# Kernel tuning notes

Measured on AMD Instinct MI355X. Metric: run time of the kernel, lower is better.

## Reference

```python
import jax, jax.numpy as jnp
import numpy as np

B, T, C = 8, 1024, 1024
NH, HD = 16, 64          # num_heads, head_dim (C = NH*HD)
NL = 8                   # num_layers
TPB = 64                 # tokens_per_block (block_causal)
EPS = 1e-5


def setup_inputs() -> dict:
    key = jax.random.key(0)
    ks = jax.random.split(key, 12)
    s = 0.02
    sequences = jax.random.normal(ks[0], (B, T, C), dtype=jnp.float32)
    # block-causal mask: causal OR same-block (tril | block_diag)
    idx = jnp.arange(T)
    mask = (idx[:, None] >= idx[None, :]) | ((idx[:, None] // TPB) == (idx[None, :] // TPB))
    # stacked per-layer params; torch Linear convention: W has shape [out, in]
    d = {
        "sequences": sequences,
        "mask": mask,
        "Wq": jax.random.normal(ks[1], (NL, C, C)) * s, "bq": jnp.zeros((NL, C)),
        "Wk": jax.random.normal(ks[2], (NL, C, C)) * s, "bk": jnp.zeros((NL, C)),
        "Wv": jax.random.normal(ks[3], (NL, C, C)) * s, "bv": jnp.zeros((NL, C)),
        "Wo": jax.random.normal(ks[4], (NL, C, C)) * s, "bo": jnp.zeros((NL, C)),
        "ln1w": jnp.ones((NL, C)), "ln1b": jnp.zeros((NL, C)),
        "ln2w": jnp.ones((NL, C)), "ln2b": jnp.zeros((NL, C)),
        "W1": jax.random.normal(ks[5], (NL, 4 * C, C)) * s, "b1": jnp.zeros((NL, 4 * C)),
        "W2": jax.random.normal(ks[6], (NL, C, 4 * C)) * s, "b2": jnp.zeros((NL, C)),
        "lnfw": jnp.ones((C,)), "lnfb": jnp.zeros((C,)),
    }
    return d


def _layernorm(x, w, b):
    m = jnp.mean(x, axis=-1, keepdims=True)
    v = jnp.mean(jnp.square(x - m), axis=-1, keepdims=True)
    return (x - m) * jax.lax.rsqrt(v + EPS) * w + b


def _linear(x, W, b):  # x: [..., in], W: [out, in]
    return jnp.einsum('...i,oi->...o', x, W) + b


def _attention(h, mask, Wq, bq, Wk, bk, Wv, bv, Wo, bo):
    # h: [B,T,C]
    q = _linear(h, Wq, bq).reshape(B, T, NH, HD)
    k = _linear(h, Wk, bk).reshape(B, T, NH, HD)
    v = _linear(h, Wv, bv).reshape(B, T, NH, HD)
    att = jnp.einsum('bqhd,bkhd->bhqk', q, k) * (HD ** -0.5)
    att = jnp.where(mask, att, -jnp.inf)
    att = jax.nn.softmax(att, axis=-1)
    y = jnp.einsum('bhqk,bkhd->bqhd', att, v).reshape(B, T, C)
    return _linear(y, Wo, bo)


def reference(sequences, mask, Wq, bq, Wk, bk, Wv, bv, Wo, bo,
              ln1w, ln1b, ln2w, ln2b, W1, b1, W2, b2, lnfw, lnfb):
    x = sequences  # dropout p=0
    for i in range(NL):
        h = _layernorm(x, ln1w[i], ln1b[i])
        x = x + _attention(h, mask, Wq[i], bq[i], Wk[i], bk[i], Wv[i], bv[i], Wo[i], bo[i])
        h = _layernorm(x, ln2w[i], ln2b[i])
        h = _linear(h, W1[i], b1[i])
        h = jax.nn.gelu(h, approximate=False)  # torch nn.GELU default = exact erf
        x = x + _linear(h, W2[i], b2[i])
    return _layernorm(x, lnfw, lnfb)
```

## Files before the change

kernel.cpp:

```cpp
#include <hip/hip_runtime.h>
#include <math.h>

typedef unsigned short ushort_t;
typedef __attribute__((ext_vector_type(4))) float f32x4;
typedef __attribute__((ext_vector_type(8))) short short8;

constexpr int BATCH = 8, T = 1024, C = 1024, NH = 16, HD = 64, NL = 8;
constexpr int MROWS = BATCH * T;
constexpr int CS = 3 * C;

#define WAITVM(n) asm volatile("s_waitcnt vmcnt(" #n ")" ::: "memory")

__device__ __forceinline__ ushort_t f2bf(float f) {
  unsigned u = __builtin_bit_cast(unsigned, f);
  u += 0x7fffu + ((u >> 16) & 1u);
  return (ushort_t)(u >> 16);
}

__device__ __forceinline__ void gload_lds16(const ushort_t* g, ushort_t* l) {
  __builtin_amdgcn_global_load_lds(
      (const __attribute__((address_space(1))) unsigned int*)g,
      (__attribute__((address_space(3))) unsigned int*)l, 16, 0, 0);
}

__global__ __launch_bounds__(256, 8)
void convw_kernel(const float* __restrict__ Wq, const float* __restrict__ Wk,
                  const float* __restrict__ Wv, const float* __restrict__ Wo,
                  const float* __restrict__ W1, const float* __restrict__ W2,
                  const float* __restrict__ bq, const float* __restrict__ bk,
                  const float* __restrict__ bv,
                  ushort_t* __restrict__ wqkv, ushort_t* __restrict__ wo,
                  ushort_t* __restrict__ w1, ushort_t* __restrict__ w2,
                  float* __restrict__ bqkv)
{
  if (blockIdx.x == 6144) {
    int t = threadIdx.x;
    if (t < 384) {
      const float* s = (t < 128) ? (bq + t * 8)
                     : (t < 256) ? (bk + (t - 128) * 8)
                                 : (bv + (t - 256) * 8);
      f32x4 a = ((const f32x4*)s)[0], b = ((const f32x4*)s)[1];
      ((f32x4*)(bqkv + t * 8))[0] = a;
      ((f32x4*)(bqkv + t * 8))[1] = b;
    }
    return;
  }
  int g = blockIdx.x * 256 + threadIdx.x;
  const float* src;
  ushort_t* dst;
  if (g < 393216) {
    int which = g >> 17;
    int r = g & 131071;
    src = (which == 0 ? Wq : which == 1 ? Wk : Wv) + (size_t)r * 8;
    dst = wqkv + (size_t)g * 8;
  } else if (g < 524288) {
    int r = g - 393216;
    src = Wo + (size_t)r * 8; dst = wo + (size_t)r * 8;
  } else if (g < 1048576) {
    int r = g - 524288;
    src = W1 + (size_t)r * 8; dst = w1 + (size_t)r * 8;
  } else {
    int r = g - 1048576;
    src = W2 + (size_t)r * 8; dst = w2 + (size_t)r * 8;
  }
  f32x4 a = ((const f32x4*)src)[0], b = ((const f32x4*)src)[1];
  short8 o;
#pragma unroll
  for (int e = 0; e < 4; ++e) { o[e] = (short)f2bf(a[e]); o[e + 4] = (short)f2bf(b[e]); }
  *(short8*)dst = o;
}

template<int MODE, int NB>
__global__ __launch_bounds__(512, 1)
void gemmk(const ushort_t* __restrict__ A, const ushort_t* __restrict__ Wb,
           const float* __restrict__ bias, ushort_t* __restrict__ outb,
           float* __restrict__ resid, int K, int N, int nbn)
{
  constexpr int MI = (NB == 256) ? 8 : 4;
  constexpr int NI = 4;
  constexpr int WAVE_M = MI * 16;
  constexpr int NBJ = (NB == 256) ? 2 : 1;
  constexpr int AT = 256 * 32;
  constexpr int BT = NB * 32;

  __shared__ __align__(16) ushort_t As[4 * AT];
  __shared__ __align__(16) ushort_t Bs[4 * BT];

  const int tid = threadIdx.x;
  const int lane = tid & 63, wave = tid >> 6;
  const int wm = (NB == 256) ? (wave >> 2) : (wave >> 1);
  const int wn = (NB == 256) ? (wave & 3) : (wave & 1);
  const int l15 = lane & 15, l4 = lane >> 4;

  const int cpx = gridDim.x >> 3;
  const int xcd = blockIdx.x & 7;
  const int local = blockIdx.x >> 3;
  const int bm = xcd * 4 + local / nbn;
  const int bn = local % nbn;
  const long bm0 = (long)bm * 256;
  const long bn0 = (long)bn * NB;

  const ushort_t* srcA[2]; int dA[2];
#pragma unroll
  for (int j = 0; j < 2; ++j) {
    int cidx = j * 512 + tid;
    int row = cidx >> 2, c = cidx & 3;
    int cl = (c - (row >> 1)) & 3;
    srcA[j] = A + (size_t)(bm0 + row) * K + cl * 8;
    dA[j] = cidx * 8;
  }
  const ushort_t* srcB[NBJ]; int dB[NBJ];
#pragma unroll
  for (int j = 0; j < NBJ; ++j) {
    int cidx = j * 512 + tid;
    int row = cidx >> 2, c = cidx & 3;
    int cl = (c - (row >> 1)) & 3;
    srcB[j] = Wb + (size_t)(bn0 + row) * K + cl * 8;
    dB[j] = cidx * 8;
  }

  int aoff[MI], boff[NI];
#pragma unroll
  for (int mi = 0; mi < MI; ++mi) {
    int row = wm * WAVE_M + mi * 16 + l15;
    int p = (l4 + (row >> 1)) & 3;
    aoff[mi] = row * 32 + p * 8;
  }
#pragma unroll
  for (int ni = 0; ni < NI; ++ni) {
    int row = wn * 64 + ni * 16 + l15;
    int p = (l4 + (row >> 1)) & 3;
    boff[ni] = row * 32 + p * 8;
  }

  auto stage = [&](int buf, int kt) {
#pragma unroll
    for (int j = 0; j < 2; ++j)
      gload_lds16(srcA[j] + kt, &As[buf * AT + dA[j]]);
#pragma unroll
    for (int j = 0; j < NBJ; ++j)
      gload_lds16(srcB[j] + kt, &Bs[buf * BT + dB[j]]);
  };

  f32x4 acc[MI][NI] = {};
  const int nt = K >> 5;

  stage(0, 0); stage(1, 32); stage(2, 64);
  if (NB == 256) WAITVM(8); else WAITVM(6);
  __builtin_amdgcn_s_barrier();

  for (int t = 0; t < nt; ++t) {
    const ushort_t* Ab = &As[(t & 3) * AT];
    const ushort_t* Bb = &Bs[(t & 3) * BT];
    short8 af[MI], bf[NI];
#pragma unroll
    for (int mi = 0; mi < MI; ++mi) af[mi] = *(const short8*)&Ab[aoff[mi]];
#pragma unroll
    for (int ni = 0; ni < NI; ++ni) bf[ni] = *(const short8*)&Bb[boff[ni]];

    if (t + 3 < nt) stage((t + 3) & 3, (t + 3) << 5);
    __builtin_amdgcn_sched_barrier(0);

    __builtin_amdgcn_s_setprio(1);
#pragma unroll
    for (int mi = 0; mi < MI; ++mi)
#pragma unroll
      for (int ni = 0; ni < NI; ++ni)
        acc[mi][ni] = __builtin_amdgcn_mfma_f32_16x16x32_bf16(
            af[mi], bf[ni], acc[mi][ni], 0, 0, 0);
    __builtin_amdgcn_s_setprio(0);

    const int rem2 = nt - 2 - t;
    if (rem2 >= 2)      { if (NB == 256) WAITVM(8); else WAITVM(6); }
    else if (rem2 == 1) { if (NB == 256) WAITVM(4); else WAITVM(3); }
    else if (rem2 == 0) { WAITVM(0); }
    __builtin_amdgcn_s_barrier();
  }

#pragma unroll
  for (int ni = 0; ni < NI; ++ni) {
    long col = bn0 + wn * 64 + ni * 16 + l15;
    float bv = bias[col];
#pragma unroll
    for (int mi = 0; mi < MI; ++mi) {
#pragma unroll
      for (int r = 0; r < 4; ++r) {
        long row = bm0 + wm * WAVE_M + mi * 16 + l4 * 4 + r;
        float v = acc[mi][ni][r] + bv;
        if (MODE == 1) v = 0.5f * v * (1.0f + erff(v * 0.70710678118f));
        if (MODE == 2) {
          float* rp = resid + (size_t)row * N + col;
          *rp = *rp + v;
        } else {
          outb[(size_t)row * N + col] = f2bf(v);
        }
      }
    }
  }
}

__global__ __launch_bounds__(256, 4)
void attn_kernel(const ushort_t* __restrict__ qkv, ushort_t* __restrict__ y)
{
  __shared__ __align__(16) ushort_t Qs[64 * 64];
  __shared__ __align__(16) ushort_t Ks[64 * 64];
  __shared__ __align__(16) ushort_t Vts[64 * 64];
  __shared__ __align__(16) ushort_t Ps[64 * 64];
  const int tid = threadIdx.x;
  const int lane = tid & 63, wave = tid >> 6;
  const int l15 = lane & 15, l4 = lane >> 4;
  const int w16 = wave * 16;
  const int bid = blockIdx.x;
  const int pair = bid & 127, qb = bid >> 7;
  const int h = pair & 15, b = pair >> 4;
  const int qoff = h * HD, koff = C + h * HD, voff = 2 * C + h * HD;
  const size_t qrow0 = (size_t)(b * T + qb * 64);

#pragma unroll
  for (int j = 0; j < 2; ++j) {
    int cidx = j * 256 + tid;
    int row = cidx >> 3, cl = (cidx & 7) ^ (row & 7);
    gload_lds16(qkv + (qrow0 + row) * CS + qoff + cl * 8, &Qs[cidx * 8]);
  }

  f32x4 o[4] = {};
  float mrun[4] = {-INFINITY, -INFINITY, -INFINITY, -INFINITY};
  float lrun[4] = {0.f, 0.f, 0.f, 0.f};

  __syncthreads();

  for (int kvb = 0; kvb <= qb; ++kvb) {
    const size_t krow0 = (size_t)(b * T + kvb * 64);
#pragma unroll
    for (int j = 0; j < 2; ++j) {
      int cidx = j * 256 + tid;
      int row = cidx >> 3, cl = (cidx & 7) ^ (row & 7);
      gload_lds16(qkv + (krow0 + row) * CS + koff + cl * 8, &Ks[cidx * 8]);
    }
#pragma unroll
    for (int pass = 0; pass < 2; ++pass) {
      int dc = (tid >> 6) + pass * 4;
      int kvr = tid & 63;
      const ushort_t* src = qkv + (krow0 + kvr) * CS + voff + dc * 8;
      short8 vv = *(const short8*)src;
#pragma unroll
      for (int i = 0; i < 8; ++i) {
        int d = dc * 8 + i;
        Vts[d * 64 + (((kvr >> 3) ^ (d & 7)) << 3) + (kvr & 7)] = (ushort_t)vv[i];
      }
    }
    __syncthreads();

    f32x4 s[4] = {};
#pragma unroll
    for (int ks = 0; ks < 2; ++ks) {
      int arow = w16 + l15;
      int pa = (ks * 4 + l4) ^ (arow & 7);
      short8 aq = *(const short8*)&Qs[arow * 64 + pa * 8];
#pragma unroll
      for (int n = 0; n < 4; ++n) {
        int br = n * 16 + l15;
        int pb = (ks * 4 + l4) ^ (br & 7);
        short8 bk2 = *(const short8*)&Ks[br * 64 + pb * 8];
        s[n] = __builtin_amdgcn_mfma_f32_16x16x32_bf16(aq, bk2, s[n], 0, 0, 0);
      }
    }

#pragma unroll
    for (int r = 0; r < 4; ++r) {
      float mx = fmaxf(fmaxf(s[0][r], s[1][r]), fmaxf(s[2][r], s[3][r]));
#pragma unroll
      for (int d = 1; d < 16; d <<= 1) mx = fmaxf(mx, __shfl_xor(mx, d, 16));
      mx *= 0.125f;
      float mnew = fmaxf(mrun[r], mx);
      float alpha = __expf(mrun[r] - mnew);
      float rowsum = 0.f;
      int qr = w16 + l4 * 4 + r;
#pragma unroll
      for (int n = 0; n < 4; ++n) {
        float pv = __expf(s[n][r] * 0.125f - mnew);
        rowsum += pv;
        int kv = n * 16 + l15;
        Ps[qr * 64 + (((kv >> 3) ^ (qr & 7)) << 3) + (kv & 7)] = f2bf(pv);
      }
#pragma unroll
      for (int d = 1; d < 16; d <<= 1) rowsum += __shfl_xor(rowsum, d, 16);
      mrun[r] = mnew;
      lrun[r] = lrun[r] * alpha + rowsum;
      o[0][r] *= alpha; o[1][r] *= alpha; o[2][r] *= alpha; o[3][r] *= alpha;
    }

#pragma unroll
    for (int ks = 0; ks < 2; ++ks) {
      int arow = w16 + l15;
      int pa = (ks * 4 + l4) ^ (arow & 7);
      short8 ap = *(const short8*)&Ps[arow * 64 + pa * 8];
#pragma unroll
      for (int n = 0; n < 4; ++n) {
        int vr = n * 16 + l15;
        int pb = (ks * 4 + l4) ^ (vr & 7);
        short8 bvv = *(const short8*)&Vts[vr * 64 + pb * 8];
        o[n] = __builtin_amdgcn_mfma_f32_16x16x32_bf16(ap, bvv, o[n], 0, 0, 0);
      }
    }
    __syncthreads();
  }

#pragma unroll
  for (int n = 0; n < 4; ++n) {
#pragma unroll
    for (int r = 0; r < 4; ++r) {
      float val = o[n][r] / lrun[r];
      y[(qrow0 + w16 + l4 * 4 + r) * C + h * HD + n * 16 + l15] = f2bf(val);
    }
  }
}

template<int OUTBF16>
__global__ __launch_bounds__(256, 4)
void ln_kernel(const float* __restrict__ x, const float* __restrict__ w,
               const float* __restrict__ bprm, void* __restrict__ out)
{
  const size_t row = blockIdx.x;
  const int tid = threadIdx.x;
  f32x4 xv = ((const f32x4*)(x + row * 1024))[tid];
  float s1 = xv[0] + xv[1] + xv[2] + xv[3];
  float s2 = xv[0] * xv[0] + xv[1] * xv[1] + xv[2] * xv[2] + xv[3] * xv[3];
#pragma unroll
  for (int m = 1; m < 64; m <<= 1) {
    s1 += __shfl_xor(s1, m);
    s2 += __shfl_xor(s2, m);
  }
  __shared__ float red[8];
  const int wave = tid >> 6, lane = tid & 63;
  if (lane == 0) { red[wave * 2] = s1; red[wave * 2 + 1] = s2; }
  __syncthreads();
  s1 = red[0] + red[2] + red[4] + red[6];
  s2 = red[1] + red[3] + red[5] + red[7];
  const float mean = s1 * (1.f / 1024.f);
  const float var = s2 * (1.f / 1024.f) - mean * mean;
  const float rstd = rsqrtf(var + 1e-5f);
  f32x4 wv = ((const f32x4*)w)[tid];
  f32x4 bv = ((const f32x4*)bprm)[tid];
  f32x4 ov;
#pragma unroll
  for (int c2 = 0; c2 < 4; ++c2) ov[c2] = (xv[c2] - mean) * rstd * wv[c2] + bv[c2];
  if (OUTBF16) {
    ushort4 u;
    u.x = f2bf(ov[0]); u.y = f2bf(ov[1]); u.z = f2bf(ov[2]); u.w = f2bf(ov[3]);
    ((ushort4*)out)[row * 256 + tid] = u;
  } else {
    ((f32x4*)out)[row * 256 + tid] = ov;
  }
}

extern "C" void kernel_launch(void* const* d_in, const int* in_sizes, int n_in,
                              void* d_out, int out_size, void* d_ws, size_t ws_size,
                              hipStream_t stream)
{
  const float* seq  = (const float*)d_in[0];
  const float* Wq   = (const float*)d_in[2];  const float* bq = (const float*)d_in[3];
  const float* Wk   = (const float*)d_in[4];  const float* bk = (const float*)d_in[5];
  const float* Wv   = (const float*)d_in[6];  const float* bv = (const float*)d_in[7];
  const float* Wo   = (const float*)d_in[8];  const float* bo = (const float*)d_in[9];
  const float* ln1w = (const float*)d_in[10]; const float* ln1b = (const float*)d_in[11];
  const float* ln2w = (const float*)d_in[12]; const float* ln2b = (const float*)d_in[13];
  const float* W1   = (const float*)d_in[14]; const float* b1 = (const float*)d_in[15];
  const float* W2   = (const float*)d_in[16]; const float* b2 = (const float*)d_in[17];
  const float* lnfw = (const float*)d_in[18]; const float* lnfb = (const float*)d_in[19];

  char* ws = (char*)d_ws;
  size_t off = 0;
  float* X = (float*)(ws + off);         off += (size_t)MROWS * C * 4;
  ushort_t* Hb = (ushort_t*)(ws + off);  off += (size_t)MROWS * C * 2;
  ushort_t* Yb = (ushort_t*)(ws + off);  off += (size_t)MROWS * C * 2;
  ushort_t* BIG = (ushort_t*)(ws + off); off += (size_t)MROWS * 4 * C * 2;
  ushort_t* wqkv = (ushort_t*)(ws + off); off += (size_t)3 * C * C * 2;
  ushort_t* wo   = (ushort_t*)(ws + off); off += (size_t)C * C * 2;
  ushort_t* w1   = (ushort_t*)(ws + off); off += (size_t)4 * C * C * 2;
  ushort_t* w2   = (ushort_t*)(ws + off); off += (size_t)4 * C * C * 2;
  float* bqkv = (float*)(ws + off);       off += (size_t)3 * C * 4;
  ushort_t* QKVb = BIG;
  ushort_t* Gb = BIG;

  hipMemcpyAsync(X, seq, (size_t)MROWS * C * 4, hipMemcpyDeviceToDevice, stream);

  const dim3 blk(256);
  const dim3 blk512(512);
  const dim3 gQKV(384);
  const dim3 gN1024(256);
  const dim3 gN4096(512);
  const dim3 gAttn(2048);
  const dim3 gConv(6145);

  for (int i = 0; i < NL; ++i) {
    const size_t w1Off = (size_t)i * C * C;
    const size_t w4Off = (size_t)i * 4 * C * C;
    convw_kernel<<<gConv, blk, 0, stream>>>(Wq + w1Off, Wk + w1Off, Wv + w1Off,
                                            Wo + w1Off, W1 + w4Off, W2 + w4Off,
                                            bq + i * C, bk + i * C, bv + i * C,
                                            wqkv, wo, w1, w2, bqkv);
    ln_kernel<1><<<MROWS, blk, 0, stream>>>(X, ln1w + i * C, ln1b + i * C, Hb);
    gemmk<0, 256><<<gQKV, blk512, 0, stream>>>(Hb, wqkv, bqkv, QKVb, nullptr, C, CS, 12);
    attn_kernel<<<gAttn, blk, 0, stream>>>(QKVb, Yb);
    gemmk<2, 128><<<gN1024, blk512, 0, stream>>>(Yb, wo, bo + i * C, nullptr, X, C, C, 8);
    ln_kernel<1><<<MROWS, blk, 0, stream>>>(X, ln2w + i * C, ln2b + i * C, Hb);
    gemmk<1, 256><<<gN4096, blk512, 0, stream>>>(Hb, w1, b1 + (size_t)i * 4 * C, Gb, nullptr, C, 4 * C, 16);
    gemmk<2, 128><<<gN1024, blk512, 0, stream>>>(Gb, w2, b2 + i * C, nullptr, X, 4 * C, C, 8);
  }
  ln_kernel<0><<<MROWS, blk, 0, stream>>>(X, lnfw, lnfb, (float*)d_out);
}
```

Measured before the change: 3.200 ms.

## Restructure GEMM into 8-phase ping-pong pipeline with LDS-staged vectorized epilogue

Replaces the 4-stage single-phase GEMM loop with a K=64 double-buffered schedule split into four interleaved load/MFMA phases separated by barriers and priority hints, so LDS reads, global-to-LDS staging and MFMA overlap more finely. Tiles change to 256-wide N with BM of 128 or 256, and occupancy is raised to 2 blocks per CU. The epilogue now transposes accumulators through LDS to emit 16-byte vectorized stores and residual updates instead of scalar strided writes. The extra barriers add synchronisation overhead, and the larger LDS footprint and register pressure may limit the intended occupancy.

```diff
diff --git a/kernel.cpp b/kernel.cpp
--- a/kernel.cpp
+++ b/kernel.cpp
@@ -9,7 +9,9 @@
 constexpr int MROWS = BATCH * T;
 constexpr int CS = 3 * C;
 
-#define WAITVM(n) asm volatile("s_waitcnt vmcnt(" #n ")" ::: "memory")
+#define WAITVM0 asm volatile("s_waitcnt vmcnt(0)" ::: "memory")
+#define WAITVM4 asm volatile("s_waitcnt vmcnt(4)" ::: "memory")
+#define WAITVM6 asm volatile("s_waitcnt vmcnt(6)" ::: "memory")
 
 __device__ __forceinline__ ushort_t f2bf(float f) {
   unsigned u = __builtin_bit_cast(unsigned, f);
@@ -70,48 +72,47 @@
   *(short8*)dst = o;
 }
 
-template<int MODE, int NB>
-__global__ __launch_bounds__(512, 1)
-void gemmk(const ushort_t* __restrict__ A, const ushort_t* __restrict__ Wb,
-           const float* __restrict__ bias, ushort_t* __restrict__ outb,
-           float* __restrict__ resid, int K, int N, int nbn)
+template<int MODE, int BM>
+__global__ __launch_bounds__(512, 2)
+void gemm8p(const ushort_t* __restrict__ A, const ushort_t* __restrict__ Wb,
+            const float* __restrict__ bias, ushort_t* __restrict__ outb,
+            float* __restrict__ resid, int K, int N, int nbn)
 {
-  constexpr int MI = (NB == 256) ? 8 : 4;
-  constexpr int NI = 4;
-  constexpr int WAVE_M = MI * 16;
-  constexpr int NBJ = (NB == 256) ? 2 : 1;
-  constexpr int AT = 256 * 32;
-  constexpr int BT = NB * 32;
-
-  __shared__ __align__(16) ushort_t As[4 * AT];
-  __shared__ __align__(16) ushort_t Bs[4 * BT];
+  constexpr int MI = BM / 32;
+  constexpr int LA = BM / 128;
+  constexpr int AKH = BM * 32;
+  constexpr int ABUF = 2 * AKH;
+  constexpr int BKH = 256 * 32;
+  constexpr int BBUF = 2 * BKH;
+  constexpr int BMT = 8192 / BM;
+
+  __shared__ __align__(16) ushort_t As[2 * ABUF];
+  __shared__ __align__(16) ushort_t Bs[2 * BBUF];
 
   const int tid = threadIdx.x;
   const int lane = tid & 63, wave = tid >> 6;
-  const int wm = (NB == 256) ? (wave >> 2) : (wave >> 1);
-  const int wn = (NB == 256) ? (wave & 3) : (wave & 1);
+  const int wm = wave >> 2, wn = wave & 3;
   const int l15 = lane & 15, l4 = lane >> 4;
 
-  const int cpx = gridDim.x >> 3;
   const int xcd = blockIdx.x & 7;
   const int local = blockIdx.x >> 3;
-  const int bm = xcd * 4 + local / nbn;
+  const int bm = xcd * (BMT / 8) + local / nbn;
   const int bn = local % nbn;
-  const long bm0 = (long)bm * 256;
-  const long bn0 = (long)bn * NB;
-
-  const ushort_t* srcA[2]; int dA[2];
-#pragma unroll
-  for (int j = 0; j < 2; ++j) {
+  const long bm0 = (long)bm * BM;
+  const long bn0 = (long)bn * 256;
+
+  const ushort_t* srcA[LA]; int dA[LA];
+#pragma unroll
+  for (int j = 0; j < LA; ++j) {
     int cidx = j * 512 + tid;
     int row = cidx >> 2, c = cidx & 3;
     int cl = (c - (row >> 1)) & 3;
     srcA[j] = A + (size_t)(bm0 + row) * K + cl * 8;
     dA[j] = cidx * 8;
   }
-  const ushort_t* srcB[NBJ]; int dB[NBJ];
-#pragma unroll
-  for (int j = 0; j < NBJ; ++j) {
+  const ushort_t* srcB[2]; int dB[2];
+#pragma unroll
+  for (int j = 0; j < 2; ++j) {
     int cidx = j * 512 + tid;
     int row = cidx >> 2, c = cidx & 3;
     int cl = (c - (row >> 1)) & 3;
@@ -119,81 +120,156 @@
     dB[j] = cidx * 8;
   }
 
-  int aoff[MI], boff[NI];
+  auto stage_unit = [&](int u) {
+    int tau = u >> 2, part = u & 3;
+    int buf = tau & 1, kh = part >> 1;
+    int kt = (tau << 6) + (kh << 5);
+    if (part & 1) {
+#pragma unroll
+      for (int j = 0; j < 2; ++j)
+        gload_lds16(srcB[j] + kt, &Bs[buf * BBUF + kh * BKH + dB[j]]);
+    } else {
+#pragma unroll
+      for (int j = 0; j < LA; ++j)
+        gload_lds16(srcA[j] + kt, &As[buf * ABUF + kh * AKH + dA[j]]);
+    }
+  };
+
+  int aoffs[MI], boffs[4];
 #pragma unroll
   for (int mi = 0; mi < MI; ++mi) {
-    int row = wm * WAVE_M + mi * 16 + l15;
-    int p = (l4 + (row >> 1)) & 3;
-    aoff[mi] = row * 32 + p * 8;
-  }
-#pragma unroll
-  for (int ni = 0; ni < NI; ++ni) {
+    int row = wm * (BM / 2) + mi * 16 + l15;
+    aoffs[mi] = row * 32 + ((l4 + (row >> 1)) & 3) * 8;
+  }
+#pragma unroll
+  for (int ni = 0; ni < 4; ++ni) {
     int row = wn * 64 + ni * 16 + l15;
-    int p = (l4 + (row >> 1)) & 3;
-    boff[ni] = row * 32 + p * 8;
-  }
-
-  auto stage = [&](int buf, int kt) {
-#pragma unroll
-    for (int j = 0; j < 2; ++j)
-      gload_lds16(srcA[j] + kt, &As[buf * AT + dA[j]]);
-#pragma unroll
-    for (int j = 0; j < NBJ; ++j)
-      gload_lds16(srcB[j] + kt, &Bs[buf * BT + dB[j]]);
-  };
-
-  f32x4 acc[MI][NI] = {};
-  const int nt = K >> 5;
-
-  stage(0, 0); stage(1, 32); stage(2, 64);
-  if (NB == 256) WAITVM(8); else WAITVM(6);
+    boffs[ni] = row * 32 + ((l4 + (row >> 1)) & 3) * 8;
+  }
+
+  f32x4 acc[MI][4] = {};
+  const int nt = K >> 6;
+  const int NU = nt << 2;
+
+#pragma unroll
+  for (int u = 0; u < 7; ++u) if (u < NU) stage_unit(u);
+  if constexpr (BM == 256) WAITVM6; else WAITVM4;
   __builtin_amdgcn_s_barrier();
+  __builtin_amdgcn_sched_barrier(0);
 
   for (int t = 0; t < nt; ++t) {
-    const ushort_t* Ab = &As[(t & 3) * AT];
-    const ushort_t* Bb = &Bs[(t & 3) * BT];
-    short8 af[MI], bf[NI];
-#pragma unroll
-    for (int mi = 0; mi < MI; ++mi) af[mi] = *(const short8*)&Ab[aoff[mi]];
-#pragma unroll
-    for (int ni = 0; ni < NI; ++ni) bf[ni] = *(const short8*)&Bb[boff[ni]];
-
-    if (t + 3 < nt) stage((t + 3) & 3, (t + 3) << 5);
-    __builtin_amdgcn_sched_barrier(0);
-
+    const int buf = t & 1;
+    const ushort_t* Ab = &As[buf * ABUF];
+    const ushort_t* Bb = &Bs[buf * BBUF];
+    short8 af[MI], bfr[4];
+
+#pragma unroll
+    for (int mi = 0; mi < MI; ++mi) af[mi] = *(const short8*)&Ab[aoffs[mi]];
+    bfr[0] = *(const short8*)&Bb[boffs[0]];
+    bfr[1] = *(const short8*)&Bb[boffs[1]];
+    if (7 + 4 * t < NU) stage_unit(7 + 4 * t);
+    __builtin_amdgcn_s_barrier();
+    __builtin_amdgcn_sched_barrier(0);
     __builtin_amdgcn_s_setprio(1);
 #pragma unroll
-    for (int mi = 0; mi < MI; ++mi)
-#pragma unroll
-      for (int ni = 0; ni < NI; ++ni)
-        acc[mi][ni] = __builtin_amdgcn_mfma_f32_16x16x32_bf16(
-            af[mi], bf[ni], acc[mi][ni], 0, 0, 0);
+    for (int mi = 0; mi < MI; ++mi) {
+      acc[mi][0] = __builtin_amdgcn_mfma_f32_16x16x32_bf16(af[mi], bfr[0], acc[mi][0], 0, 0, 0);
+      acc[mi][1] = __builtin_amdgcn_mfma_f32_16x16x32_bf16(af[mi], bfr[1], acc[mi][1], 0, 0, 0);
+    }
     __builtin_amdgcn_s_setprio(0);
-
-    const int rem2 = nt - 2 - t;
-    if (rem2 >= 2)      { if (NB == 256) WAITVM(8); else WAITVM(6); }
-    else if (rem2 == 1) { if (NB == 256) WAITVM(4); else WAITVM(3); }
-    else if (rem2 == 0) { WAITVM(0); }
-    __builtin_amdgcn_s_barrier();
-  }
-
-#pragma unroll
-  for (int ni = 0; ni < NI; ++ni) {
-    long col = bn0 + wn * 64 + ni * 16 + l15;
-    float bv = bias[col];
+    __builtin_amdgcn_s_barrier();
+    __builtin_amdgcn_sched_barrier(0);
+
+    bfr[2] = *(const short8*)&Bb[boffs[2]];
+    bfr[3] = *(const short8*)&Bb[boffs[3]];
+    if (8 + 4 * t < NU) stage_unit(8 + 4 * t);
+    __builtin_amdgcn_s_barrier();
+    __builtin_amdgcn_sched_barrier(0);
+    __builtin_amdgcn_s_setprio(1);
 #pragma unroll
     for (int mi = 0; mi < MI; ++mi) {
-#pragma unroll
-      for (int r = 0; r < 4; ++r) {
-        long row = bm0 + wm * WAVE_M + mi * 16 + l4 * 4 + r;
-        float v = acc[mi][ni][r] + bv;
-        if (MODE == 1) v = 0.5f * v * (1.0f + erff(v * 0.70710678118f));
-        if (MODE == 2) {
-          float* rp = resid + (size_t)row * N + col;
-          *rp = *rp + v;
-        } else {
-          outb[(size_t)row * N + col] = f2bf(v);
+      acc[mi][2] = __builtin_amdgcn_mfma_f32_16x16x32_bf16(af[mi], bfr[2], acc[mi][2], 0, 0, 0);
+      acc[mi][3] = __builtin_amdgcn_mfma_f32_16x16x32_bf16(af[mi], bfr[3], acc[mi][3], 0, 0, 0);
+    }
+    __builtin_amdgcn_s_setprio(0);
+    __builtin_amdgcn_s_barrier();
+    __builtin_amdgcn_sched_barrier(0);
+
+#pragma unroll
+    for (int mi = 0; mi < MI; ++mi) af[mi] = *(const short8*)&Ab[AKH + aoffs[mi]];
+    bfr[0] = *(const short8*)&Bb[BKH + boffs[0]];
+    bfr[1] = *(const short8*)&Bb[BKH + boffs[1]];
+    if (9 + 4 * t < NU) stage_unit(9 + 4 * t);
+    __builtin_amdgcn_s_barrier();
+    __builtin_amdgcn_sched_barrier(0);
+    __builtin_amdgcn_s_setprio(1);
+#pragma unroll
+    for (int mi = 0; mi < MI; ++mi) {
+      acc[mi][0] = __builtin_amdgcn_mfma_f32_16x16x32_bf16(af[mi], bfr[0], acc[mi][0], 0, 0, 0);
+      acc[mi][1] = __builtin_amdgcn_mfma_f32_16x16x32_bf16(af[mi], bfr[1], acc[mi][1], 0, 0, 0);
+    }
+    __builtin_amdgcn_s_setprio(0);
+    __builtin_amdgcn_s_barrier();
+    __builtin_amdgcn_sched_barrier(0);
+
+    bfr[2] = *(const short8*)&Bb[BKH + boffs[2]];
+    bfr[3] = *(const short8*)&Bb[BKH + boffs[3]];
+    if (10 + 4 * t < NU) stage_unit(10 + 4 * t);
+    if (t < nt - 2) { if constexpr (BM == 256) WAITVM6; else WAITVM4; }
+    else if (t == nt - 2) { WAITVM0; }
+    __builtin_amdgcn_s_barrier();
+    __builtin_amdgcn_sched_barrier(0);
+    __builtin_amdgcn_s_setprio(1);
+#pragma unroll
+    for (int mi = 0; mi < MI; ++mi) {
+      acc[mi][2] = __builtin_amdgcn_mfma_f32_16x16x32_bf16(af[mi], bfr[2], acc[mi][2], 0, 0, 0);
+      acc[mi][3] = __builtin_amdgcn_mfma_f32_16x16x32_bf16(af[mi], bfr[3], acc[mi][3], 0, 0, 0);
+    }
+    __builtin_amdgcn_s_setprio(0);
+    __builtin_amdgcn_s_barrier();
+    __builtin_amdgcn_sched_barrier(0);
+  }
+
+  float* fl = (float*)&Bs[0] + wave * (16 * 68);
+  const long grow0 = bm0 + wm * (BM / 2);
+  const long gcol0 = bn0 + wn * 64;
+  const int c8 = lane & 7;
+  const f32x4 bb0 = *(const f32x4*)&bias[gcol0 + c8 * 8];
+  const f32x4 bb1 = *(const f32x4*)&bias[gcol0 + c8 * 8 + 4];
+
+#pragma unroll
+  for (int mi = 0; mi < MI; ++mi) {
+#pragma unroll
+    for (int ni = 0; ni < 4; ++ni)
+#pragma unroll
+      for (int r = 0; r < 4; ++r)
+        fl[(l4 * 4 + r) * 68 + ni * 16 + l15] = acc[mi][ni][r];
+#pragma unroll
+    for (int pass = 0; pass < 2; ++pass) {
+      int row = pass * 8 + (lane >> 3);
+      f32x4 v0 = *(const f32x4*)&fl[row * 68 + c8 * 8];
+      f32x4 v1 = *(const f32x4*)&fl[row * 68 + c8 * 8 + 4];
+      v0 += bb0; v1 += bb1;
+      const long grow = grow0 + mi * 16 + row;
+      if (MODE == 1) {
+#pragma unroll
+        for (int e = 0; e < 4; ++e) {
+          v0[e] = 0.5f * v0[e] * (1.0f + erff(v0[e] * 0.70710678118f));
+          v1[e] = 0.5f * v1[e] * (1.0f + erff(v1[e] * 0.70710678118f));
         }
+      }
+      if (MODE == 2) {
+        float* rp = resid + (size_t)grow * N + gcol0 + c8 * 8;
+        f32x4 r0 = *(const f32x4*)rp;
+        f32x4 r1 = *(const f32x4*)(rp + 4);
+        r0 += v0; r1 += v1;
+        *(f32x4*)rp = r0;
+        *(f32x4*)(rp + 4) = r1;
+      } else {
+        short8 o;
+#pragma unroll
+        for (int e = 0; e < 4; ++e) { o[e] = (short)f2bf(v0[e]); o[e + 4] = (short)f2bf(v1[e]); }
+        *(short8*)&outb[(size_t)grow * N + gcol0 + c8 * 8] = o;
       }
     }
   }
@@ -388,8 +464,9 @@
   const dim3 blk(256);
   const dim3 blk512(512);
   const dim3 gQKV(384);
-  const dim3 gN1024(256);
-  const dim3 gN4096(512);
+  const dim3 gWo(256);
+  const dim3 gW1(512);
+  const dim3 gW2(256);
   const dim3 gAttn(2048);
   const dim3 gConv(6145);
 
@@ -401,12 +478,12 @@
                                             bq + i * C, bk + i * C, bv + i * C,
                                             wqkv, wo, w1, w2, bqkv);
     ln_kernel<1><<<MROWS, blk, 0, stream>>>(X, ln1w + i * C, ln1b + i * C, Hb);
-    gemmk<0, 256><<<gQKV, blk512, 0, stream>>>(Hb, wqkv, bqkv, QKVb, nullptr, C, CS, 12);
+    gemm8p<0, 256><<<gQKV, blk512, 0, stream>>>(Hb, wqkv, bqkv, QKVb, nullptr, C, CS, 12);
     attn_kernel<<<gAttn, blk, 0, stream>>>(QKVb, Yb);
-    gemmk<2, 128><<<gN1024, blk512, 0, stream>>>(Yb, wo, bo + i * C, nullptr, X, C, C, 8);
+    gemm8p<2, 128><<<gWo, blk512, 0, stream>>>(Yb, wo, bo + i * C, nullptr, X, C, C, 4);
     ln_kernel<1><<<MROWS, blk, 0, stream>>>(X, ln2w + i * C, ln2b + i * C, Hb);
-    gemmk<1, 256><<<gN4096, blk512, 0, stream>>>(Hb, w1, b1 + (size_t)i * 4 * C, Gb, nullptr, C, 4 * C, 16);
-    gemmk<2, 128><<<gN1024, blk512, 0, stream>>>(Gb, w2, b2 + i * C, nullptr, X, 4 * C, C, 8);
+    gemm8p<1, 256><<<gW1, blk512, 0, stream>>>(Hb, w1, b1 + (size_t)i * 4 * C, Gb, nullptr, C, 4 * C, 16);
+    gemm8p<2, 128><<<gW2, blk512, 0, stream>>>(Gb, w2, b2 + i * C, nullptr, X, 4 * C, C, 4);
   }
   ln_kernel<0><<<MROWS, blk, 0, stream>>>(X, lnfw, lnfb, (float*)d_out);
 }
```

Result: no change. 3.181 ms (-0.6%).
